# Kernel optimization log

Measured on AMD Instinct MI355X. Metric: run time of the kernel, lower is better.

The kernel has to match this reference:

```python
import jax, jax.numpy as jnp
import numpy as np

N_USERS = 10000
RESERVE = 100
N_TOTAL = N_USERS + RESERVE  # 10100 graph nodes (incl. unknown-user slots)
D = 128                      # user_id_embedding_size
B = 2048                     # batch of user ids
AVG_DEG = 32


def _build_friendship_matrix(rng: np.random.Generator) -> np.ndarray:
    # Dense symmetric friendship matrix with 1.0 on the diagonal (self-loop),
    # mirroring torch.diag(ones) + symmetric weighted edge insertion.
    F = np.zeros((N_TOTAL, N_TOTAL), dtype=np.float32)
    np.fill_diagonal(F, 1.0)
    n_edges = N_USERS * AVG_DEG // 2
    src = rng.integers(0, N_USERS, size=n_edges)
    dst = rng.integers(0, N_USERS, size=n_edges)
    w = rng.uniform(0.1, 1.0, size=n_edges).astype(np.float32)
    F[src, dst] = w
    F[dst, src] = w
    return F


def setup_inputs() -> dict:
    key = jax.random.key(0)
    k_ids, k_emb, k_w, k_b = jax.random.split(key, 4)
    rng = np.random.default_rng(0)
    user_ids = jax.random.randint(k_ids, (B,), 0, N_USERS, dtype=jnp.int32)
    friendship_matrix = jnp.asarray(_build_friendship_matrix(rng))      # (N, N)
    # torch init: embeddings ~ U[0,1); Linear weight/bias ~ U[-1/sqrt(d), 1/sqrt(d)]
    user_id_embeddings = jax.random.uniform(k_emb, (N_TOTAL, D), dtype=jnp.float32)
    bound = 1.0 / np.sqrt(D)
    lin_weight = jax.random.uniform(k_w, (D, D), minval=-bound, maxval=bound, dtype=jnp.float32)
    lin_bias = jax.random.uniform(k_b, (D,), minval=-bound, maxval=bound, dtype=jnp.float32)
    return {
        "user_ids": user_ids,
        "friendship_matrix": friendship_matrix,
        "user_id_embeddings": user_id_embeddings,
        "lin_weight": lin_weight,
        "lin_bias": lin_bias,
    }


def reference(user_ids, friendship_matrix, user_id_embeddings, lin_weight, lin_bias):
    # Per user: friends = F[uid]; aggregated = sum_n friends[n] * E[n]
    # Vectorized over the batch: gather rows of F, then one GEMM with E.
    friends = friendship_matrix[user_ids]                 # (B, N)
    aggregated = friends @ user_id_embeddings             # (B, D)
    # torch.nn.Linear: x @ W^T + b
    return aggregated @ lin_weight.T + lin_bias           # (B, D)
```

## Files before the change

### kernel.cpp

```cpp
#include <hip/hip_runtime.h>


#define NTOT 10100
#define NV4  2525
#define QV4  632
#define DIM  128
#define WCAP 80
#define TPB  256

__global__ __launch_bounds__(TPB) void friendship_kernel(
    const int*   __restrict__ uids,
    const float* __restrict__ F,
    const float* __restrict__ E,
    const float* __restrict__ W,
    const float* __restrict__ bias,
    float*       __restrict__ out)
{
    __shared__ int   s_idx[4][WCAP];
    __shared__ float s_w[4][WCAP];
    __shared__ float s_part[4][DIM];
    __shared__ float s_agg[DIM];
    __shared__ float s_out[DIM];

    const int row  = blockIdx.x;
    const int tid  = threadIdx.x;
    const int w    = tid >> 6;
    const int lane = tid & 63;
    const int uid  = uids[row];
    const float* Frow = F + (size_t)uid * NTOT;
    const float4* Frow4 = (const float4*)Frow;

    const int jbeg = w * QV4;
    const int jend = (w == 3) ? NV4 : (jbeg + QV4);
    const unsigned long long below = (1ULL << lane) - 1ULL;
    const int nrounds = (jend - jbeg + 63) >> 6;

    int cb = 0;
    for (int t = 0; t < nrounds; ++t) {
        const int j = jbeg + t * 64 + lane;
        float4 v = make_float4(0.f, 0.f, 0.f, 0.f);
        if (j < jend) v = Frow4[j];
        bool b0 = v.x != 0.0f, b1 = v.y != 0.0f, b2 = v.z != 0.0f, b3 = v.w != 0.0f;
        unsigned long long m0 = __ballot(b0), m1 = __ballot(b1);
        unsigned long long m2 = __ballot(b2), m3 = __ballot(b3);
        if (m0 | m1 | m2 | m3) {
            int t0 = __popcll(m0), t1 = __popcll(m1), t2 = __popcll(m2);
            int n = j * 4;
            int p0 = cb + __popcll(m0 & below);
            int p1 = cb + t0 + __popcll(m1 & below);
            int p2 = cb + t0 + t1 + __popcll(m2 & below);
            int p3 = cb + t0 + t1 + t2 + __popcll(m3 & below);
            if (b0 && p0 < WCAP) { s_idx[w][p0] = n;     s_w[w][p0] = v.x; }
            if (b1 && p1 < WCAP) { s_idx[w][p1] = n + 1; s_w[w][p1] = v.y; }
            if (b2 && p2 < WCAP) { s_idx[w][p2] = n + 2; s_w[w][p2] = v.z; }
            if (b3 && p3 < WCAP) { s_idx[w][p3] = n + 3; s_w[w][p3] = v.w; }
            cb += t0 + t1 + t2 + __popcll(m3);
        }
    }
    asm volatile("s_waitcnt lgkmcnt(0)" ::: "memory");
    __builtin_amdgcn_sched_barrier(0);

    float2 acc = make_float2(0.0f, 0.0f);
    const float* Ed = E + 2 * lane;
    if (cb <= WCAP) {
        int k = 0;
        for (; k + 4 <= cb; k += 4) {
            int   n0 = s_idx[w][k],     n1 = s_idx[w][k + 1];
            int   n2 = s_idx[w][k + 2], n3 = s_idx[w][k + 3];
            float w0 = s_w[w][k],       w1 = s_w[w][k + 1];
            float w2 = s_w[w][k + 2],   w3 = s_w[w][k + 3];
            float2 e0 = *(const float2*)(Ed + (size_t)n0 * DIM);
            float2 e1 = *(const float2*)(Ed + (size_t)n1 * DIM);
            float2 e2 = *(const float2*)(Ed + (size_t)n2 * DIM);
            float2 e3 = *(const float2*)(Ed + (size_t)n3 * DIM);
            acc.x += w0 * e0.x; acc.y += w0 * e0.y;
            acc.x += w1 * e1.x; acc.y += w1 * e1.y;
            acc.x += w2 * e2.x; acc.y += w2 * e2.y;
            acc.x += w3 * e3.x; acc.y += w3 * e3.y;
        }
        for (; k < cb; ++k) {
            int   n = s_idx[w][k];
            float ww = s_w[w][k];
            float2 ev = *(const float2*)(Ed + (size_t)n * DIM);
            acc.x += ww * ev.x; acc.y += ww * ev.y;
        }
    } else {
        int nbeg = jbeg * 4, nend = (w == 3) ? NTOT : (jend * 4);
        for (int n = nbeg; n < nend; ++n) {
            float fw = Frow[n];
            if (fw != 0.0f) {
                float2 ev = *(const float2*)(Ed + (size_t)n * DIM);
                acc.x += fw * ev.x; acc.y += fw * ev.y;
            }
        }
    }
    *(float2*)&s_part[w][2 * lane] = acc;
    __syncthreads();

    if (tid < DIM)
        s_agg[tid] = s_part[0][tid] + s_part[1][tid] + s_part[2][tid] + s_part[3][tid];
    __syncthreads();

    const float4* W4 = (const float4*)W;
    #pragma unroll
    for (int q = 0; q < 16; ++q) {
        int i4 = tid + TPB * q;
        float4 wv = W4[i4];
        int j  = i4 >> 5;
        int dd = (i4 & 31) * 4;
        float4 ag = *(const float4*)&s_agg[dd];
        float p = wv.x * ag.x + wv.y * ag.y + wv.z * ag.z + wv.w * ag.w;
        p += __shfl_xor(p, 16);
        p += __shfl_xor(p, 8);
        p += __shfl_xor(p, 4);
        p += __shfl_xor(p, 2);
        p += __shfl_xor(p, 1);
        if ((tid & 31) == 0) s_out[j] = p;
    }
    __syncthreads();
    if (tid < DIM)
        out[(size_t)row * DIM + tid] = bias[tid] + s_out[tid];
}

extern "C" void kernel_launch(void* const* d_in, const int* in_sizes, int n_in,
                              void* d_out, int out_size, void* d_ws, size_t ws_size,
                              hipStream_t stream) {
    const int*   uids = (const int*)  d_in[0];
    const float* F    = (const float*)d_in[1];
    const float* E    = (const float*)d_in[2];
    const float* W    = (const float*)d_in[3];
    const float* bias = (const float*)d_in[4];
    float*       out  = (float*)d_out;

    const int B = in_sizes[0];
    friendship_kernel<<<B, TPB, 0, stream>>>(uids, F, E, W, bias, out);
}
```

Baseline: 37.06 us.

## Stream friendship row into LDS asynchronously and compact nonzeros via LDS atomics

Each wave issues all ten of its row-chunk loads up front with global_load_lds, so the F row goes straight into shared memory. It then drains the chunks one at a time with staged vmcnt waits, overlapping memory latency with the nonzero scan. Compaction now uses per-wave LDS atomic counters instead of four ballots plus popcounts, which makes the order of the compacted list nondeterministic. The per-wave list capacity goes up to 96, and the partition changes to 640 float4 per wave, with indices clamped at the row end.

```diff
diff --git a/kernel.cpp b/kernel.cpp
--- a/kernel.cpp
+++ b/kernel.cpp
@@ -3,10 +3,25 @@
 
 #define NTOT 10100
 #define NV4  2525
-#define QV4  632
 #define DIM  128
-#define WCAP 80
 #define TPB  256
+#define NRND 10
+#define WCAP 96
+
+__device__ __forceinline__ void wait_vmcnt(int n) {
+    switch (n) {
+        case 0: asm volatile("s_waitcnt vmcnt(0)" ::: "memory"); break;
+        case 1: asm volatile("s_waitcnt vmcnt(1)" ::: "memory"); break;
+        case 2: asm volatile("s_waitcnt vmcnt(2)" ::: "memory"); break;
+        case 3: asm volatile("s_waitcnt vmcnt(3)" ::: "memory"); break;
+        case 4: asm volatile("s_waitcnt vmcnt(4)" ::: "memory"); break;
+        case 5: asm volatile("s_waitcnt vmcnt(5)" ::: "memory"); break;
+        case 6: asm volatile("s_waitcnt vmcnt(6)" ::: "memory"); break;
+        case 7: asm volatile("s_waitcnt vmcnt(7)" ::: "memory"); break;
+        case 8: asm volatile("s_waitcnt vmcnt(8)" ::: "memory"); break;
+        default: asm volatile("s_waitcnt vmcnt(9)" ::: "memory"); break;
+    }
+}
 
 __global__ __launch_bounds__(TPB) void friendship_kernel(
     const int*   __restrict__ uids,
@@ -16,8 +31,10 @@
     const float* __restrict__ bias,
     float*       __restrict__ out)
 {
+    __shared__ __align__(16) float4 s_row[4 * NRND * 64];
     __shared__ int   s_idx[4][WCAP];
     __shared__ float s_w[4][WCAP];
+    __shared__ int   s_cnt[4];
     __shared__ float s_part[4][DIM];
     __shared__ float s_agg[DIM];
     __shared__ float s_out[DIM];
@@ -30,41 +47,51 @@
     const float* Frow = F + (size_t)uid * NTOT;
     const float4* Frow4 = (const float4*)Frow;
 
-    const int jbeg = w * QV4;
-    const int jend = (w == 3) ? NV4 : (jbeg + QV4);
-    const unsigned long long below = (1ULL << lane) - 1ULL;
-    const int nrounds = (jend - jbeg + 63) >> 6;
+    if (lane == 0) s_cnt[w] = 0;
 
-    int cb = 0;
-    for (int t = 0; t < nrounds; ++t) {
-        const int j = jbeg + t * 64 + lane;
-        float4 v = make_float4(0.f, 0.f, 0.f, 0.f);
-        if (j < jend) v = Frow4[j];
-        bool b0 = v.x != 0.0f, b1 = v.y != 0.0f, b2 = v.z != 0.0f, b3 = v.w != 0.0f;
-        unsigned long long m0 = __ballot(b0), m1 = __ballot(b1);
-        unsigned long long m2 = __ballot(b2), m3 = __ballot(b3);
-        if (m0 | m1 | m2 | m3) {
-            int t0 = __popcll(m0), t1 = __popcll(m1), t2 = __popcll(m2);
-            int n = j * 4;
-            int p0 = cb + __popcll(m0 & below);
-            int p1 = cb + t0 + __popcll(m1 & below);
-            int p2 = cb + t0 + t1 + __popcll(m2 & below);
-            int p3 = cb + t0 + t1 + t2 + __popcll(m3 & below);
-            if (b0 && p0 < WCAP) { s_idx[w][p0] = n;     s_w[w][p0] = v.x; }
-            if (b1 && p1 < WCAP) { s_idx[w][p1] = n + 1; s_w[w][p1] = v.y; }
-            if (b2 && p2 < WCAP) { s_idx[w][p2] = n + 2; s_w[w][p2] = v.z; }
-            if (b3 && p3 < WCAP) { s_idx[w][p3] = n + 3; s_w[w][p3] = v.w; }
-            cb += t0 + t1 + t2 + __popcll(m3);
+    asm volatile("s_waitcnt vmcnt(0)" ::: "memory");
+
+    #pragma unroll
+    for (int t = 0; t < NRND; ++t) {
+        int j  = 640 * w + 64 * t + lane;
+        int jc = (j < NV4) ? j : (NV4 - 1);
+        __builtin_amdgcn_global_load_lds(
+            (const __attribute__((address_space(1))) void*)(Frow4 + jc),
+            (__attribute__((address_space(3))) void*)&s_row[(w * NRND + t) * 64],
+            16, 0, 0);
+    }
+
+    #pragma unroll
+    for (int t = 0; t < NRND; ++t) {
+        wait_vmcnt(NRND - 1 - t);
+        __builtin_amdgcn_sched_barrier(0);
+        float4 vv = s_row[(w * NRND + t) * 64 + lane];
+        int i = 640 * w + 64 * t + lane;
+        if (i < NV4) {
+            int n = i * 4;
+            bool ba = vv.x != 0.0f, bb = vv.y != 0.0f, bc = vv.z != 0.0f, bd = vv.w != 0.0f;
+            int  m  = (int)ba + (int)bb + (int)bc + (int)bd;
+            if (m) {
+                int p = atomicAdd(&s_cnt[w], m);
+                if (p + m <= WCAP) {
+                    if (ba) { s_idx[w][p] = n;     s_w[w][p] = vv.x; ++p; }
+                    if (bb) { s_idx[w][p] = n + 1; s_w[w][p] = vv.y; ++p; }
+                    if (bc) { s_idx[w][p] = n + 2; s_w[w][p] = vv.z; ++p; }
+                    if (bd) { s_idx[w][p] = n + 3; s_w[w][p] = vv.w; ++p; }
+                }
+            }
         }
     }
     asm volatile("s_waitcnt lgkmcnt(0)" ::: "memory");
     __builtin_amdgcn_sched_barrier(0);
 
+    const int cnt = s_cnt[w];
+
     float2 acc = make_float2(0.0f, 0.0f);
     const float* Ed = E + 2 * lane;
-    if (cb <= WCAP) {
+    if (cnt <= WCAP) {
         int k = 0;
-        for (; k + 4 <= cb; k += 4) {
+        for (; k + 4 <= cnt; k += 4) {
             int   n0 = s_idx[w][k],     n1 = s_idx[w][k + 1];
             int   n2 = s_idx[w][k + 2], n3 = s_idx[w][k + 3];
             float w0 = s_w[w][k],       w1 = s_w[w][k + 1];
@@ -78,14 +105,15 @@
             acc.x += w2 * e2.x; acc.y += w2 * e2.y;
             acc.x += w3 * e3.x; acc.y += w3 * e3.y;
         }
-        for (; k < cb; ++k) {
-            int   n = s_idx[w][k];
+        for (; k < cnt; ++k) {
+            int   n  = s_idx[w][k];
             float ww = s_w[w][k];
             float2 ev = *(const float2*)(Ed + (size_t)n * DIM);
             acc.x += ww * ev.x; acc.y += ww * ev.y;
         }
     } else {
-        int nbeg = jbeg * 4, nend = (w == 3) ? NTOT : (jend * 4);
+        const int nbeg = 2560 * w;
+        const int nend = (w == 3) ? NTOT : 2560 * (w + 1);
         for (int n = nbeg; n < nend; ++n) {
             float fw = Frow[n];
             if (fw != 0.0f) {
```

Measured after the change: 43.17 us. 1.16x slower.
